# Kernel tuning notes

Measured on AMD Instinct MI355X. Metric: run time of the kernel, lower is better.

## Reference

```python
import jax, jax.numpy as jnp
import numpy as np

B, T, C = 16, 2048, 384
E = 8          # num_experts
TOP_K = 2
CAP_F = 1.0
D_FF = 4 * C   # 1536


def setup_inputs() -> dict:
    key = jax.random.key(0)
    ks = jax.random.split(key, 10)
    s = 0.02
    return {
        "x": jax.random.normal(ks[0], (B, T, C), dtype=jnp.float32),
        "noise": jax.random.normal(ks[1], (B, T, E), dtype=jnp.float32),
        "w_route": jax.random.normal(ks[2], (C, E), dtype=jnp.float32) * s,
        "b_route": jnp.zeros((E,), dtype=jnp.float32),
        "w_noise": jax.random.normal(ks[3], (C, E), dtype=jnp.float32) * s,
        "b_noise": jnp.zeros((E,), dtype=jnp.float32),
        "w1": jax.random.normal(ks[4], (E, C, D_FF), dtype=jnp.float32) * s,
        "b1": jnp.zeros((E, D_FF), dtype=jnp.float32),
        "w2": jax.random.normal(ks[5], (E, D_FF, C), dtype=jnp.float32) * s,
        "b2": jnp.zeros((E, C), dtype=jnp.float32),
    }


def _moe_forward(x, noise, w_route, b_route, w_noise, b_noise, w1, b1, w2, b2):
    Bx, Tx, Cx = x.shape
    N = Bx * Tx
    cap = int(N * TOP_K / E * CAP_F)  # static expert capacity

    # --- NoisyTopkRouter ---
    logits = jnp.einsum('btc,ce->bte', x, w_route) + b_route
    noise_logits = jnp.einsum('btc,ce->bte', x, w_noise) + b_noise
    noisy = logits + noise * jax.nn.softplus(noise_logits)
    topv, topi = jax.lax.top_k(noisy, TOP_K)                    # [B,T,K]
    keep_mask = jnp.any(jax.nn.one_hot(topi, E, dtype=jnp.bool_), axis=-2)  # [B,T,E]
    sparse_logits = jnp.where(keep_mask, noisy, -jnp.inf)
    gating = jax.nn.softmax(sparse_logits, axis=-1)             # [B,T,E]

    # --- dispatch by top-1 expert with capacity drop (eval: dropout off) ---
    flat_x = x.reshape(N, Cx)
    flat_g = gating.reshape(N, E)
    top1 = jnp.argmax(flat_g, axis=-1)                          # [N]
    token_ids = jnp.arange(N, dtype=jnp.int32)
    out = jnp.zeros_like(flat_x)

    for i in range(E):
        mask = top1 == i                                        # [N]
        pos = jnp.cumsum(mask) - 1                              # rank within expert
        keep = mask & (pos < cap)
        slot = jnp.where(keep, pos, cap)                        # overflow -> dummy slot
        buf = jnp.zeros((cap + 1,), dtype=jnp.int32).at[slot].set(token_ids)
        idx = buf[:cap]                                         # token id per capacity slot
        valid = (jnp.arange(cap) < jnp.sum(keep))[:, None]      # [cap,1]
        xi = flat_x[idx]                                        # [cap,C] gather
        h = jnp.square(jax.nn.relu(xi @ w1[i] + b1[i]))         # ReLU^2
        yi = h @ w2[i] + b2[i]                                  # [cap,C]
        weighted = yi * flat_g[idx, i][:, None] * valid
        out = out.at[idx].add(weighted)                         # scatter-add

    return out.reshape(Bx, Tx, Cx)


def reference(x, noise, w_route, b_route, w_noise, b_noise, w1, b1, w2, b2):
    return _moe_forward(x, noise, w_route, b_route, w_noise, b_noise, w1, b1, w2, b2)
```

## Files before the change

kernel.cpp:

```cpp
#include <hip/hip_runtime.h>
#include <stdint.h>

#define E_NUM 8
#define CAP 8192
#define NTOK 32768
#define CDIM 384
#define DFF 1536
#define CNT_PAD 64

typedef unsigned short u16;
typedef __attribute__((ext_vector_type(8))) short short8;
typedef __attribute__((ext_vector_type(4))) float f32x4;

__device__ inline u16 f2bf(float f) {
    uint32_t u = __builtin_bit_cast(uint32_t, f);
    u += 0x7fffu + ((u >> 16) & 1u);
    return (u16)(u >> 16);
}

__device__ inline void gload_lds16(const void* g, void* l) {
    __builtin_amdgcn_global_load_lds(
        (const __attribute__((address_space(1))) void*)(uintptr_t)g,
        (__attribute__((address_space(3))) void*)(uint32_t)(uintptr_t)l,
        16, 0, 0);
}

__device__ inline float rsum_to_halves(float v) {
    int s;
    s = __builtin_bit_cast(int, v);
    v += __builtin_bit_cast(float, __builtin_amdgcn_update_dpp(0, s, 0x121, 0xF, 0xF, false));
    s = __builtin_bit_cast(int, v);
    v += __builtin_bit_cast(float, __builtin_amdgcn_update_dpp(0, s, 0x122, 0xF, 0xF, false));
    s = __builtin_bit_cast(int, v);
    v += __builtin_bit_cast(float, __builtin_amdgcn_update_dpp(0, s, 0x124, 0xF, 0xF, false));
    s = __builtin_bit_cast(int, v);
    v += __builtin_bit_cast(float, __builtin_amdgcn_update_dpp(0, s, 0x128, 0xF, 0xF, false));
    s = __builtin_bit_cast(int, v);
    v += __builtin_bit_cast(float, __builtin_amdgcn_ds_swizzle(s, 0x401F));
    return v;
}

__device__ inline float lane_total(float v) {
    int s = __builtin_bit_cast(int, v);
    return __builtin_bit_cast(float, __builtin_amdgcn_readlane(s, 0)) +
           __builtin_bit_cast(float, __builtin_amdgcn_readlane(s, 32));
}

__device__ inline void expert_span(const int* __restrict__ cnt, int e,
                                   int& base, int& n_e) {
    base = 0; n_e = 0;
#pragma unroll
    for (int i = 0; i < E_NUM; ++i) {
        int n = min(cnt[i * CNT_PAD], CAP);
        if (i < e) base += (n + 127) & ~127;
        else if (i == e) n_e = n;
    }
}

__global__ __launch_bounds__(256, 1) void routing_kernel(
    const float* __restrict__ x, const float* __restrict__ noise,
    const float* __restrict__ w_route, const float* __restrict__ b_route,
    const float* __restrict__ w_noise, const float* __restrict__ b_noise,
    int* __restrict__ cnt, int* __restrict__ list, float* __restrict__ gate,
    u16* __restrict__ xbf)
{
    __shared__ int s_top1[16];
    int lane = threadIdx.x & 63, w = threadIdx.x >> 6;
    float4 wr4[12], wn4[12];
#pragma unroll
    for (int i = 0; i < 6; ++i) {
        const float4* pr = (const float4*)(w_route + (size_t)(lane + 64 * i) * 8);
        const float4* pn = (const float4*)(w_noise + (size_t)(lane + 64 * i) * 8);
        wr4[2 * i] = pr[0]; wr4[2 * i + 1] = pr[1];
        wn4[2 * i] = pn[0]; wn4[2 * i + 1] = pn[1];
    }
    float br[E_NUM], bn[E_NUM];
#pragma unroll
    for (int e = 0; e < E_NUM; ++e) { br[e] = b_route[e]; bn[e] = b_noise[e]; }

    int tbase = blockIdx.x * 16 + w * 4;
#pragma unroll
    for (int tt = 0; tt < 4; ++tt) {
        int t = tbase + tt;
        const float* xr = x + (size_t)t * CDIM;
        float xv[6];
#pragma unroll
        for (int i = 0; i < 6; ++i) xv[i] = xr[lane + i * 64];
        u16* xb = xbf + (size_t)t * CDIM;
#pragma unroll
        for (int i = 0; i < 6; ++i) xb[lane + i * 64] = f2bf(xv[i]);
        float ar[E_NUM], an[E_NUM];
#pragma unroll
        for (int e = 0; e < E_NUM; ++e) { ar[e] = 0.f; an[e] = 0.f; }
#pragma unroll
        for (int i = 0; i < 6; ++i) {
            float4 r0 = wr4[2 * i], r1 = wr4[2 * i + 1];
            float4 n0 = wn4[2 * i], n1 = wn4[2 * i + 1];
            float xi = xv[i];
            ar[0] += xi * r0.x; ar[1] += xi * r0.y; ar[2] += xi * r0.z; ar[3] += xi * r0.w;
            ar[4] += xi * r1.x; ar[5] += xi * r1.y; ar[6] += xi * r1.z; ar[7] += xi * r1.w;
            an[0] += xi * n0.x; an[1] += xi * n0.y; an[2] += xi * n0.z; an[3] += xi * n0.w;
            an[4] += xi * n1.x; an[5] += xi * n1.y; an[6] += xi * n1.z; an[7] += xi * n1.w;
        }
        float nz[E_NUM];
        const float* np = noise + (size_t)t * E_NUM;
#pragma unroll
        for (int e = 0; e < E_NUM; ++e) {
            float sr = lane_total(rsum_to_halves(ar[e])) + br[e];
            float sn = lane_total(rsum_to_halves(an[e])) + bn[e];
            float sp = fmaxf(sn, 0.f) + __logf(1.f + __expf(-fabsf(sn)));
            nz[e] = sr + np[e] * sp;
        }
        float v1 = -1e30f; int i1 = 0;
#pragma unroll
        for (int e = 0; e < E_NUM; ++e) if (nz[e] > v1) { v1 = nz[e]; i1 = e; }
        float v2 = -1e30f;
#pragma unroll
        for (int e = 0; e < E_NUM; ++e) if (e != i1 && nz[e] > v2) v2 = nz[e];
        if (lane == 0) {
            gate[t] = 1.f / (1.f + __expf(v2 - v1));
            s_top1[w * 4 + tt] = i1;
        }
    }
    __syncthreads();
    if (w == 0) {
        int tok = blockIdx.x * 16 + lane;
        int e1 = (lane < 16) ? s_top1[lane] : -1;
#pragma unroll
        for (int e = 0; e < E_NUM; ++e) {
            unsigned long long m = __ballot(e1 == e);
            if (m == 0) continue;
            int c = __popcll(m);
            int leader = __ffsll((long long)m) - 1;
            int basec = 0;
            if (lane == leader) basec = atomicAdd(&cnt[e * CNT_PAD], c);
            basec = __shfl(basec, leader);
            if (e1 == e) {
                int pos = basec + __popcll(m & ((1ull << lane) - 1ull));
                if (pos < CAP) list[e * CAP + pos] = tok;
            }
        }
    }
}

__global__ __launch_bounds__(256) void transpose_cvt_kernel(
    const float* __restrict__ w1, u16* __restrict__ W1t,
    const float* __restrict__ w2, u16* __restrict__ W2t)
{
    __shared__ float tile[32][33];
    int z = blockIdx.z;
    const float* in; u16* out; int R, S, r0, c0;
    if (z < E_NUM) {
        in = w1 + (size_t)z * CDIM * DFF;  out = W1t + (size_t)z * CDIM * DFF;
        R = CDIM; S = DFF;
        c0 = blockIdx.x * 32; r0 = blockIdx.y * 32;
    } else {
        in = w2 + (size_t)(z - E_NUM) * DFF * CDIM;
        out = W2t + (size_t)(z - E_NUM) * DFF * CDIM;
        R = DFF; S = CDIM;
        r0 = blockIdx.x * 32; c0 = blockIdx.y * 32;
    }
    int tx = threadIdx.x, ty = threadIdx.y;
#pragma unroll
    for (int i = ty; i < 32; i += 8)
        tile[i][tx] = in[(size_t)(r0 + i) * S + (c0 + tx)];
    __syncthreads();
#pragma unroll
    for (int i = ty; i < 32; i += 8)
        out[(size_t)(c0 + i) * R + (r0 + tx)] = f2bf(tile[tx][i]);
}

template <int KD, int ND, bool FFN1>
__global__ __launch_bounds__(256, 2) void gemm_kernel(
    const u16* __restrict__ A, const u16* __restrict__ Bt,
    const float* __restrict__ bias, u16* __restrict__ H, float* __restrict__ Out,
    const int* __restrict__ cnt, const int* __restrict__ list,
    const float* __restrict__ gate)
{
    constexpr int NT = ND / 128;
    int bid = blockIdx.x;
    int xcd = bid & 7, slot = bid >> 3;
    int n_idx = slot % NT;
    int mglob = xcd + 8 * (slot / NT);
    int e = mglob >> 6;
    int m0 = (mglob & 63) * 128;
    int base, n_e;
    expert_span(cnt, e, base, n_e);
    int pad_e = (n_e + 127) & ~127;
    if (m0 >= pad_e) return;
    const u16* Be = Bt + ((size_t)e * ND + (size_t)n_idx * 128) * KD;

    __shared__ __align__(16) u16 As[2][128 * 64];
    __shared__ __align__(16) u16 Bs[2][128 * 64];
    __shared__ int s_tok[128];

    int tid = threadIdx.x;
    int w = tid >> 6, lane = tid & 63;
    int quad = lane >> 4, l15 = lane & 15;
    int wr = w & 1, wc = w >> 1;

    int srow = tid >> 3;
    int gcol = ((tid & 7) ^ ((tid >> 3) & 7)) * 8;

    if (FFN1) {
        if (tid < 128) {
            int rr = m0 + tid;
            s_tok[tid] = (rr < n_e) ? list[(size_t)e * CAP + rr] : NTOK;
        }
        __syncthreads();
    }
    const u16* Arow[4];
#pragma unroll
    for (int i = 0; i < 4; ++i) {
        int row = i * 32 + srow;
        if (FFN1) Arow[i] = A + (size_t)s_tok[row] * KD;
        else      Arow[i] = A + (size_t)(base + m0 + row) * KD;
    }

    auto stage = [&](int buf, int kb) {
#pragma unroll
        for (int i = 0; i < 4; ++i) {
            gload_lds16(Arow[i] + kb * 64 + gcol, &As[buf][i * 2048 + tid * 8]);
            gload_lds16(Be + (size_t)(i * 32 + srow) * KD + kb * 64 + gcol,
                        &Bs[buf][i * 2048 + tid * 8]);
        }
    };

    f32x4 acc[4][4];
    f32x4 zero = {0.f, 0.f, 0.f, 0.f};
#pragma unroll
    for (int a = 0; a < 4; ++a)
#pragma unroll
        for (int b = 0; b < 4; ++b) acc[a][b] = zero;

    constexpr int NK = KD / 64;
    stage(0, 0);
#pragma unroll 2
    for (int kb = 0; kb < NK; ++kb) {
        const int cur = kb & 1;
        if (kb + 1 < NK) {
            stage(cur ^ 1, kb + 1);
            asm volatile("s_waitcnt vmcnt(8)" ::: "memory");
        } else {
            asm volatile("s_waitcnt vmcnt(0)" ::: "memory");
        }
        __builtin_amdgcn_s_barrier();
        __builtin_amdgcn_sched_barrier(0);
#pragma unroll
        for (int h = 0; h < 2; ++h) {
            int pga = (((h * 4 + quad) ^ (l15 & 7))) * 8;
            short8 af[4], bf[4];
#pragma unroll
            for (int t = 0; t < 4; ++t) {
                af[t] = *(const short8*)&As[cur][(wr * 64 + t * 16 + l15) * 64 + pga];
                bf[t] = *(const short8*)&Bs[cur][(wc * 64 + t * 16 + l15) * 64 + pga];
            }
#pragma unroll
            for (int mt = 0; mt < 4; ++mt)
#pragma unroll
                for (int nt = 0; nt < 4; ++nt)
                    acc[mt][nt] = __builtin_amdgcn_mfma_f32_16x16x32_bf16(
                        af[mt], bf[nt], acc[mt][nt], 0, 0, 0);
        }
        __builtin_amdgcn_sched_barrier(0);
        __builtin_amdgcn_s_barrier();
        __builtin_amdgcn_sched_barrier(0);
    }

    int n0 = n_idx * 128;
    if (FFN1) {
        u16* Hs = (u16*)&As[0][0];
#pragma unroll
        for (int mt = 0; mt < 4; ++mt) {
            int rowL = wr * 64 + mt * 16 + quad * 4;
#pragma unroll
            for (int nt = 0; nt < 4; ++nt) {
                int colL = wc * 64 + nt * 16 + l15;
                float b = bias[(size_t)e * ND + n0 + colL];
#pragma unroll
                for (int r = 0; r < 4; ++r) {
                    float v = acc[mt][nt][r] + b;
                    v = fmaxf(v, 0.f);
                    int row = rowL + r;
                    Hs[row * 128 + (colL ^ ((row & 7) << 3))] = f2bf(v * v);
                }
            }
        }
        __syncthreads();
        u16* He = H + (size_t)(base + m0) * ND + n0;
#pragma unroll
        for (int j = 0; j < 8; ++j) {
            int idx = tid + j * 256;
            int row = idx >> 4;
            int c8 = (idx & 15) * 8;
            *(f32x4*)(He + (size_t)row * ND + c8) =
                *(const f32x4*)(Hs + row * 128 + (c8 ^ ((row & 7) << 3)));
        }
    } else {
#pragma unroll
        for (int mt = 0; mt < 4; ++mt) {
            int rowL = wr * 64 + mt * 16 + quad * 4;
#pragma unroll
            for (int r = 0; r < 4; ++r) {
                int rr = m0 + rowL + r;
                if (rr < n_e) {
                    int tok = list[(size_t)e * CAP + rr];
                    float g = gate[tok];
#pragma unroll
                    for (int nt = 0; nt < 4; ++nt) {
                        int col = n0 + wc * 64 + nt * 16 + l15;
                        float v = acc[mt][nt][r] + bias[(size_t)e * ND + col];
                        Out[(size_t)tok * CDIM + col] = v * g;
                    }
                }
            }
        }
    }
}

extern "C" void kernel_launch(void* const* d_in, const int* in_sizes, int n_in,
                              void* d_out, int out_size, void* d_ws, size_t ws_size,
                              hipStream_t stream)
{
    const float* x       = (const float*)d_in[0];
    const float* noise   = (const float*)d_in[1];
    const float* w_route = (const float*)d_in[2];
    const float* b_route = (const float*)d_in[3];
    const float* w_noise = (const float*)d_in[4];
    const float* b_noise = (const float*)d_in[5];
    const float* w1      = (const float*)d_in[6];
    const float* b1      = (const float*)d_in[7];
    const float* w2      = (const float*)d_in[8];
    const float* b2      = (const float*)d_in[9];
    float* out = (float*)d_out;

    char* ws = (char*)d_ws;
    size_t off = 0;
    auto alloc = [&](size_t bytes) {
        char* p = ws + off;
        off += (bytes + 255) & ~(size_t)255;
        return p;
    };
    int*   cnt  = (int*)alloc((size_t)E_NUM * CNT_PAD * sizeof(int));
    int*   list = (int*)alloc((size_t)E_NUM * CAP * sizeof(int));
    float* gate = (float*)alloc((size_t)NTOK * sizeof(float));
    u16*   W1t  = (u16*)alloc((size_t)E_NUM * DFF * CDIM * 2);
    u16*   W2t  = (u16*)alloc((size_t)E_NUM * CDIM * DFF * 2);

    u16* Xbf = (u16*)alloc((size_t)(NTOK + 1) * CDIM * 2);
    size_t rows = NTOK + E_NUM * 128;
    u16* Hb = (u16*)alloc(rows * DFF * 2);

    hipMemsetAsync(cnt, 0, (size_t)E_NUM * CNT_PAD * sizeof(int), stream);
    hipMemsetAsync(Xbf + (size_t)NTOK * CDIM, 0, CDIM * 2, stream);

    routing_kernel<<<NTOK / 16, 256, 0, stream>>>(x, noise, w_route, b_route,
                                                  w_noise, b_noise, cnt, list, gate, Xbf);
    transpose_cvt_kernel<<<dim3(48, 12, 16), dim3(32, 8), 0, stream>>>(w1, W1t, w2, W2t);

    gemm_kernel<CDIM, DFF, true><<<dim3((DFF / 128) * 512), 256, 0, stream>>>(
        Xbf, W1t, b1, Hb, nullptr, cnt, list, nullptr);
    gemm_kernel<DFF, CDIM, false><<<dim3((CDIM / 128) * 512), 256, 0, stream>>>(
        Hb, W2t, b2, nullptr, out, cnt, list, gate);
}
```

Baseline: 315.7 us.

## Restructure routing kernel to thread-per-token with LDS-staged x tiles

Rewrites the router so each block handles 64 tokens. x is staged in LDS in 64-column chunks, with a coalesced float4 load and bf16 conversion on the way in. Each thread accumulates one token's logits over a quarter of the channels, and the four partial sums are combined through LDS, which replaces the per-token wave-wide DPP reductions. It also raises occupancy (launch bounds 4) and lets one wave do top-1 counting with ballots over 64 tokens at once. The cost is more LDS traffic and syncs, and the route/noise weights are now read per thread from global/L1 instead of sitting in registers.

```diff
diff --git a/kernel.cpp b/kernel.cpp
--- a/kernel.cpp
+++ b/kernel.cpp
@@ -25,27 +25,6 @@
         16, 0, 0);
 }
 
-__device__ inline float rsum_to_halves(float v) {
-    int s;
-    s = __builtin_bit_cast(int, v);
-    v += __builtin_bit_cast(float, __builtin_amdgcn_update_dpp(0, s, 0x121, 0xF, 0xF, false));
-    s = __builtin_bit_cast(int, v);
-    v += __builtin_bit_cast(float, __builtin_amdgcn_update_dpp(0, s, 0x122, 0xF, 0xF, false));
-    s = __builtin_bit_cast(int, v);
-    v += __builtin_bit_cast(float, __builtin_amdgcn_update_dpp(0, s, 0x124, 0xF, 0xF, false));
-    s = __builtin_bit_cast(int, v);
-    v += __builtin_bit_cast(float, __builtin_amdgcn_update_dpp(0, s, 0x128, 0xF, 0xF, false));
-    s = __builtin_bit_cast(int, v);
-    v += __builtin_bit_cast(float, __builtin_amdgcn_ds_swizzle(s, 0x401F));
-    return v;
-}
-
-__device__ inline float lane_total(float v) {
-    int s = __builtin_bit_cast(int, v);
-    return __builtin_bit_cast(float, __builtin_amdgcn_readlane(s, 0)) +
-           __builtin_bit_cast(float, __builtin_amdgcn_readlane(s, 32));
-}
-
 __device__ inline void expert_span(const int* __restrict__ cnt, int e,
                                    int& base, int& n_e) {
     base = 0; n_e = 0;
@@ -57,59 +36,88 @@
     }
 }
 
-__global__ __launch_bounds__(256, 1) void routing_kernel(
+#define RT_TOK 64
+#define RT_KC 64
+#define RT_XS 68
+
+__global__ __launch_bounds__(256, 4) void routing_kernel(
     const float* __restrict__ x, const float* __restrict__ noise,
     const float* __restrict__ w_route, const float* __restrict__ b_route,
     const float* __restrict__ w_noise, const float* __restrict__ b_noise,
     int* __restrict__ cnt, int* __restrict__ list, float* __restrict__ gate,
     u16* __restrict__ xbf)
 {
-    __shared__ int s_top1[16];
-    int lane = threadIdx.x & 63, w = threadIdx.x >> 6;
-    float4 wr4[12], wn4[12];
-#pragma unroll
-    for (int i = 0; i < 6; ++i) {
-        const float4* pr = (const float4*)(w_route + (size_t)(lane + 64 * i) * 8);
-        const float4* pn = (const float4*)(w_noise + (size_t)(lane + 64 * i) * 8);
-        wr4[2 * i] = pr[0]; wr4[2 * i + 1] = pr[1];
-        wn4[2 * i] = pn[0]; wn4[2 * i + 1] = pn[1];
-    }
-    float br[E_NUM], bn[E_NUM];
-#pragma unroll
-    for (int e = 0; e < E_NUM; ++e) { br[e] = b_route[e]; bn[e] = b_noise[e]; }
-
-    int tbase = blockIdx.x * 16 + w * 4;
-#pragma unroll
-    for (int tt = 0; tt < 4; ++tt) {
-        int t = tbase + tt;
-        const float* xr = x + (size_t)t * CDIM;
-        float xv[6];
-#pragma unroll
-        for (int i = 0; i < 6; ++i) xv[i] = xr[lane + i * 64];
-        u16* xb = xbf + (size_t)t * CDIM;
-#pragma unroll
-        for (int i = 0; i < 6; ++i) xb[lane + i * 64] = f2bf(xv[i]);
-        float ar[E_NUM], an[E_NUM];
-#pragma unroll
-        for (int e = 0; e < E_NUM; ++e) { ar[e] = 0.f; an[e] = 0.f; }
-#pragma unroll
-        for (int i = 0; i < 6; ++i) {
-            float4 r0 = wr4[2 * i], r1 = wr4[2 * i + 1];
-            float4 n0 = wn4[2 * i], n1 = wn4[2 * i + 1];
-            float xi = xv[i];
-            ar[0] += xi * r0.x; ar[1] += xi * r0.y; ar[2] += xi * r0.z; ar[3] += xi * r0.w;
-            ar[4] += xi * r1.x; ar[5] += xi * r1.y; ar[6] += xi * r1.z; ar[7] += xi * r1.w;
-            an[0] += xi * n0.x; an[1] += xi * n0.y; an[2] += xi * n0.z; an[3] += xi * n0.w;
-            an[4] += xi * n1.x; an[5] += xi * n1.y; an[6] += xi * n1.z; an[7] += xi * n1.w;
+    __shared__ float xs[RT_TOK * RT_XS];
+    int tid = threadIdx.x;
+    int lane = tid & 63;
+    int seg = __builtin_amdgcn_readfirstlane(tid >> 6);
+    int tok = tid & 63;
+    int t0 = blockIdx.x * RT_TOK;
+
+    int srow = tid >> 4;
+    int scol = (tid & 15) * 4;
+
+    float ar[E_NUM], an[E_NUM];
+#pragma unroll
+    for (int e = 0; e < E_NUM; ++e) { ar[e] = 0.f; an[e] = 0.f; }
+
+    for (int c = 0; c < CDIM / RT_KC; ++c) {
+        __syncthreads();
+#pragma unroll
+        for (int p = 0; p < 4; ++p) {
+            int row = p * 16 + srow;
+            float4 v = *(const float4*)(x + (size_t)(t0 + row) * CDIM + c * RT_KC + scol);
+            *(float4*)&xs[row * RT_XS + scol] = v;
+            uint2 b;
+            b.x = (uint32_t)f2bf(v.x) | ((uint32_t)f2bf(v.y) << 16);
+            b.y = (uint32_t)f2bf(v.z) | ((uint32_t)f2bf(v.w) << 16);
+            *(uint2*)(xbf + (size_t)(t0 + row) * CDIM + c * RT_KC + scol) = b;
+        }
+        __syncthreads();
+#pragma unroll
+        for (int q = 0; q < 4; ++q) {
+            float4 xq = *(const float4*)&xs[tok * RT_XS + seg * 16 + q * 4];
+            int kb = c * RT_KC + seg * 16 + q * 4;
+#pragma unroll
+            for (int jj = 0; jj < 4; ++jj) {
+                const float* wrk = w_route + (size_t)(kb + jj) * E_NUM;
+                const float* wnk = w_noise + (size_t)(kb + jj) * E_NUM;
+                float4 wa = *(const float4*)wrk, wb = *(const float4*)(wrk + 4);
+                float4 na = *(const float4*)wnk, nb = *(const float4*)(wnk + 4);
+                float xk = (jj == 0) ? xq.x : (jj == 1) ? xq.y : (jj == 2) ? xq.z : xq.w;
+                ar[0] += xk * wa.x; ar[1] += xk * wa.y; ar[2] += xk * wa.z; ar[3] += xk * wa.w;
+                ar[4] += xk * wb.x; ar[5] += xk * wb.y; ar[6] += xk * wb.z; ar[7] += xk * wb.w;
+                an[0] += xk * na.x; an[1] += xk * na.y; an[2] += xk * na.z; an[3] += xk * na.w;
+                an[4] += xk * nb.x; an[5] += xk * nb.y; an[6] += xk * nb.z; an[7] += xk * nb.w;
+            }
+        }
+    }
+    __syncthreads();
+    float* part = xs;
+    float* pp = part + (size_t)(seg * 64 + tok) * 16;
+    *(f32x4*)&pp[0]  = (f32x4){ar[0], ar[1], ar[2], ar[3]};
+    *(f32x4*)&pp[4]  = (f32x4){ar[4], ar[5], ar[6], ar[7]};
+    *(f32x4*)&pp[8]  = (f32x4){an[0], an[1], an[2], an[3]};
+    *(f32x4*)&pp[12] = (f32x4){an[4], an[5], an[6], an[7]};
+    __syncthreads();
+    if (seg == 0) {
+        int t = t0 + lane;
+        float sr[E_NUM], sn[E_NUM];
+#pragma unroll
+        for (int e = 0; e < E_NUM; ++e) { sr[e] = b_route[e]; sn[e] = b_noise[e]; }
+#pragma unroll
+        for (int s = 0; s < 4; ++s) {
+            const float* q = part + (size_t)(s * 64 + lane) * 16;
+#pragma unroll
+            for (int e = 0; e < E_NUM; ++e) { sr[e] += q[e]; sn[e] += q[8 + e]; }
         }
         float nz[E_NUM];
         const float* np = noise + (size_t)t * E_NUM;
 #pragma unroll
         for (int e = 0; e < E_NUM; ++e) {
-            float sr = lane_total(rsum_to_halves(ar[e])) + br[e];
-            float sn = lane_total(rsum_to_halves(an[e])) + bn[e];
-            float sp = fmaxf(sn, 0.f) + __logf(1.f + __expf(-fabsf(sn)));
-            nz[e] = sr + np[e] * sp;
+            float s = sn[e];
+            float sp = fmaxf(s, 0.f) + __logf(1.f + __expf(-fabsf(s)));
+            nz[e] = sr[e] + np[e] * sp;
         }
         float v1 = -1e30f; int i1 = 0;
 #pragma unroll
@@ -117,27 +125,19 @@
         float v2 = -1e30f;
 #pragma unroll
         for (int e = 0; e < E_NUM; ++e) if (e != i1 && nz[e] > v2) v2 = nz[e];
-        if (lane == 0) {
-            gate[t] = 1.f / (1.f + __expf(v2 - v1));
-            s_top1[w * 4 + tt] = i1;
-        }
-    }
-    __syncthreads();
-    if (w == 0) {
-        int tok = blockIdx.x * 16 + lane;
-        int e1 = (lane < 16) ? s_top1[lane] : -1;
+        gate[t] = 1.f / (1.f + __expf(v2 - v1));
 #pragma unroll
         for (int e = 0; e < E_NUM; ++e) {
-            unsigned long long m = __ballot(e1 == e);
+            unsigned long long m = __ballot(i1 == e);
             if (m == 0) continue;
-            int c = __popcll(m);
+            int cnum = __popcll(m);
             int leader = __ffsll((long long)m) - 1;
             int basec = 0;
-            if (lane == leader) basec = atomicAdd(&cnt[e * CNT_PAD], c);
+            if (lane == leader) basec = atomicAdd(&cnt[e * CNT_PAD], cnum);
             basec = __shfl(basec, leader);
-            if (e1 == e) {
+            if (i1 == e) {
                 int pos = basec + __popcll(m & ((1ull << lane) - 1ull));
-                if (pos < CAP) list[e * CAP + pos] = tok;
+                if (pos < CAP) list[e * CAP + pos] = t;
             }
         }
     }
@@ -354,8 +354,8 @@
     hipMemsetAsync(cnt, 0, (size_t)E_NUM * CNT_PAD * sizeof(int), stream);
     hipMemsetAsync(Xbf + (size_t)NTOK * CDIM, 0, CDIM * 2, stream);
 
-    routing_kernel<<<NTOK / 16, 256, 0, stream>>>(x, noise, w_route, b_route,
-                                                  w_noise, b_noise, cnt, list, gate, Xbf);
+    routing_kernel<<<NTOK / RT_TOK, 256, 0, stream>>>(x, noise, w_route, b_route,
+                                                      w_noise, b_noise, cnt, list, gate, Xbf);
     transpose_cvt_kernel<<<dim3(48, 12, 16), dim3(32, 8), 0, stream>>>(w1, W1t, w2, W2t);
 
     gemm_kernel<CDIM, DFF, true><<<dim3((DFF / 128) * 512), 256, 0, stream>>>(
```

Result: faster. 305.0 us (-3.4%).
